# Kernel tuning notes

Hardware: AMD Instinct MI355X
Metric: run time of the kernel (lower is better)

Reference implementation:

```python
import jax, jax.numpy as jnp
import numpy as np

B, L, DIN, D = 16, 1024, 512, 1024  # batch, l_max, input_dim, d_model
ORDER = 2


def setup_inputs() -> dict:
    key = jax.random.key(0)
    ks = jax.random.split(key, 8)
    n = lambda i, shape, sc: jax.random.normal(ks[i], shape, dtype=jnp.float32) * sc
    return {
        "x": n(0, (B, L, DIN), 1.0),
        # project_in (Linear since input_dim != output_dim)
        "Wp": n(1, (DIN, D), DIN ** -0.5),
        "bp": jnp.zeros((D,), jnp.float32),
        # hyena in_proj -> (order+1)*d channels
        "W_in": n(2, (D, 3 * D), D ** -0.5),
        "b_in": jnp.zeros((3 * D,), jnp.float32),
        # depthwise causal short conv, kernel 3
        "short_w": n(3, (3 * D, 1, 3), 0.5),
        "short_b": jnp.zeros((3 * D,), jnp.float32),
        # implicit long filters (materialized) + per-channel skip bias
        "k_filt": n(4, (ORDER, L, D), 0.02),
        "D_bias": n(5, (ORDER, D), 1.0),
        # hyena out_proj
        "W_out": n(6, (D, D), D ** -0.5),
        "b_out": jnp.zeros((D,), jnp.float32),
    }


def _fftconv(v, k, d_bias):
    # v: [B, L, d], k: [L, d] -> causal long conv via zero-padded FFT + skip
    n = 2 * v.shape[1]
    vf = jnp.fft.rfft(v.astype(jnp.float32), n=n, axis=1)
    kf = jnp.fft.rfft(k.astype(jnp.float32), n=n, axis=0)
    y = jnp.fft.irfft(vf * kf[None], n=n, axis=1)[:, : v.shape[1]]
    return (y + v * d_bias).astype(v.dtype)


def reference(x, Wp, bp, W_in, b_in, short_w, short_b, k_filt, D_bias, W_out, b_out):
    u = x @ Wp + bp                      # [B, L, D] project_in
    u = u @ W_in + b_in                  # [B, L, 3D]
    # depthwise causal short conv over sequence
    uc = jnp.transpose(u, (0, 2, 1))     # [B, 3D, L]
    uc = jax.lax.conv_general_dilated(
        uc, short_w, window_strides=(1,), padding=[(2, 0)],
        feature_group_count=3 * D, dimension_numbers=("NCH", "OIH", "NCH"),
    )[..., :L] + short_b[None, :, None]
    uc = jnp.transpose(uc, (0, 2, 1))    # [B, L, 3D]
    x1, x2, v = jnp.split(uc, 3, axis=-1)
    # Hyena recurrence: gate then long FFT conv, order=2
    v = _fftconv(v * x2, k_filt[0], D_bias[0])
    v = _fftconv(v * x1, k_filt[1], D_bias[1])
    return v @ W_out + b_out             # [B, L, D]
```

## Files before the change

kernel.cpp:

```cpp
#include <hip/hip_runtime.h>

#define BATCH 16
#define LSEQ 1024
#define DIN 512
#define DMODEL 1024
#define D3 3072
#define KCP 1064

typedef __attribute__((ext_vector_type(4))) float f32x4;
typedef __attribute__((ext_vector_type(8))) short bf16x8;

static __device__ __forceinline__ ushort f2bf(float f) {
    uint u = __float_as_uint(f);
    return (ushort)((u + 0x7FFFu + ((u >> 16) & 1u)) >> 16);
}
static __device__ __forceinline__ float bf2f(ushort h) {
    return __uint_as_float(((uint)h) << 16);
}

#define GLD16(ldst, gsrc)                                                        \
    __builtin_amdgcn_global_load_lds(                                            \
        (const __attribute__((address_space(1))) void*)(gsrc),                   \
        (__attribute__((address_space(3))) void*)(ldst), 16, 0, 0)

template <typename OutT, bool HAS_BIAS>
__global__ __launch_bounds__(256) void gemm_mfma(const ushort* __restrict__ A,
                                                 const ushort* __restrict__ Bt,
                                                 const float* __restrict__ bias,
                                                 OutT* __restrict__ C,
                                                 int M, int N, int K) {
    __shared__ ushort Als[2][128 * 32];
    __shared__ ushort Bls[2][128 * 32];
    int nwg = gridDim.x * gridDim.y;
    int bid = blockIdx.y * gridDim.x + blockIdx.x;
    bid = (bid & 7) * (nwg >> 3) + (bid >> 3);
    int n0 = (bid % gridDim.x) * 128, m0 = (bid / gridDim.x) * 128;
    int t = threadIdx.x;
    int w = t >> 6, l = t & 63;
    int wm = w & 1, wn = w >> 1;
    f32x4 acc[4][4] = {};

    int rowA = t >> 2;
    int kb = (t & 3) * 8;
    const ushort* gA0 = A + (size_t)(m0 + rowA) * K + kb;
    const ushort* gA1 = gA0 + (size_t)64 * K;
    const ushort* gB0 = Bt + (size_t)(n0 + rowA) * K + kb;
    const ushort* gB1 = gB0 + (size_t)64 * K;
    int so = 512 * w;

    int aoff = (wm * 64 + (l & 15)) * 32 + (l >> 4) * 8;
    int boff = (wn * 64 + (l & 15)) * 32 + (l >> 4) * 8;

    GLD16(&Als[0][so], gA0);
    GLD16(&Als[0][2048 + so], gA1);
    GLD16(&Bls[0][so], gB0);
    GLD16(&Bls[0][2048 + so], gB1);
    GLD16(&Als[1][so], gA0 + 32);
    GLD16(&Als[1][2048 + so], gA1 + 32);
    GLD16(&Bls[1][so], gB0 + 32);
    GLD16(&Bls[1][2048 + so], gB1 + 32);

    int cur = 0;
    for (int k0 = 0; k0 < K; k0 += 32) {
        if (k0 + 32 < K)
            asm volatile("s_waitcnt vmcnt(4)" ::: "memory");
        else
            asm volatile("s_waitcnt vmcnt(0)" ::: "memory");
        __builtin_amdgcn_s_barrier();
        __builtin_amdgcn_sched_barrier(0);
        bf16x8 af[4], bg[4];
#pragma unroll
        for (int i = 0; i < 4; i++) af[i] = *(const bf16x8*)&Als[cur][aoff + i * 512];
#pragma unroll
        for (int j = 0; j < 4; j++) bg[j] = *(const bf16x8*)&Bls[cur][boff + j * 512];
#pragma unroll
        for (int i = 0; i < 4; i++)
#pragma unroll
            for (int j = 0; j < 4; j++)
                acc[i][j] = __builtin_amdgcn_mfma_f32_16x16x32_bf16(af[i], bg[j],
                                                                    acc[i][j], 0, 0, 0);
        asm volatile("s_waitcnt lgkmcnt(0)" ::: "memory");
        __builtin_amdgcn_sched_barrier(0);
        __builtin_amdgcn_s_barrier();
        if (k0 + 64 < K) {
            GLD16(&Als[cur][so], gA0 + k0 + 64);
            GLD16(&Als[cur][2048 + so], gA1 + k0 + 64);
            GLD16(&Bls[cur][so], gB0 + k0 + 64);
            GLD16(&Bls[cur][2048 + so], gB1 + k0 + 64);
        }
        cur ^= 1;
    }

#pragma unroll
    for (int j = 0; j < 4; j++) {
        int col = n0 + wn * 64 + 16 * j + (l & 15);
        float bv = HAS_BIAS ? bias[col] : 0.f;
#pragma unroll
        for (int i = 0; i < 4; i++) {
            int row0 = m0 + wm * 64 + 16 * i + (l >> 4) * 4;
#pragma unroll
            for (int r = 0; r < 4; r++) {
                float v = acc[i][j][r] + bv;
                if constexpr (sizeof(OutT) == 2)
                    C[(size_t)(row0 + r) * N + col] = (OutT)f2bf(v);
                else
                    C[(size_t)(row0 + r) * N + col] = (OutT)v;
            }
        }
    }
}

__global__ __launch_bounds__(512, 2) void conv_mfma(const ushort* __restrict__ At,
                                                    const ushort* __restrict__ X1t,
                                                    const float* __restrict__ kt,
                                                    const float* __restrict__ Db,
                                                    ushort* __restrict__ V2t, int nb) {
    __shared__ ushort a_lds[16 * 1024];
    __shared__ ushort kc[8 * KCP];
    int d = blockIdx.x;
    int tid = threadIdx.x;
    int w = tid >> 6, l = tid & 63;
    int lr = l & 15, lq = l >> 4;

    {
        int b = tid >> 5, s = tid & 31;
        const ushort* g = At + ((size_t)b * DMODEL + d) * LSEQ + s * 32;
#pragma unroll
        for (int j = 0; j < 4; j++) {
            uint4 v = {0u, 0u, 0u, 0u};
            if (b < nb) v = *(const uint4*)(g + 8 * j);
            int byte = (b * 1024 + s * 32 + 8 * j) * 2;
            *(uint4*)((char*)a_lds + (byte ^ (b << 4))) = v;
        }
    }

    int p = (7 - lr) & 7;
    int v0 = 1023 - lr + 8 * lq - p;
    int a_base = lr * 2048 + lq * 16;
    int swz = lr << 4;
    int tL0 = 2 * w, tF0 = 2 * w + 1;
    int tL1 = 30 - 2 * w, tF1 = 31 - 2 * w;

#define AFB(BLK) (*(const bf16x8*)((const char*)a_lds + ((a_base + 64 * (BLK)) ^ swz)))
#define MF(AF, B, AC) AC = __builtin_amdgcn_mfma_f32_16x16x32_bf16(AF, B, AC, 0, 0, 0)

    for (int o = 0; o < 2; o++) {
        const float* krow = kt + ((size_t)o * DMODEL + d) * LSEQ;
        for (int idx = tid; idx < 8 * KCP; idx += 512) {
            int pp = idx / KCP;
            int u = idx - pp * KCP;
            int ki = 1023 - u - pp;
            kc[idx] = f2bf((ki >= 0) ? krow[ki] : 0.f);
        }
        __syncthreads();

        f32x4 aL0l = {}, aL0h = {}, aF0l = {}, aF0h = {};
        f32x4 aL1l = {}, aL1h = {}, aF1l = {}, aF1h = {};
        const char* kbp = (const char*)kc + ((size_t)p * KCP + v0) * 2;
        bf16x8 hold0, hold1;
        {
            bf16x8 b0 = *(const bf16x8*)(kbp);
            bf16x8 b1 = *(const bf16x8*)(kbp - 32);
            __builtin_amdgcn_s_setprio(1);
            bf16x8 f0 = AFB(tF0);
            MF(f0, b0, aF0l); MF(f0, b1, aF0h);
            hold0 = AFB(tL0);
            MF(hold0, b0, aL0l); MF(hold0, b1, aL0h);
            bf16x8 f1 = AFB(tF1);
            MF(f1, b0, aF1l); MF(f1, b1, aF1h);
            hold1 = AFB(tL1);
            MF(hold1, b0, aL1l); MF(hold1, b1, aL1h);
            __builtin_amdgcn_s_setprio(0);
        }
        for (int m = 1; m < 32; m++) {
            bf16x8 b0 = *(const bf16x8*)(kbp - 64 * m);
            bf16x8 b1 = *(const bf16x8*)(kbp - 64 * m - 32);
            __builtin_amdgcn_s_setprio(1);
            if (m <= tF0) { MF(hold0, b0, aF0l); MF(hold0, b1, aF0h); }
            if (m <= tL0) {
                hold0 = AFB(tL0 - m);
                MF(hold0, b0, aL0l); MF(hold0, b1, aL0h);
            }
            if (m <= tF1) { MF(hold1, b0, aF1l); MF(hold1, b1, aF1h); }
            if (m <= tL1) {
                hold1 = AFB(tL1 - m);
                MF(hold1, b0, aL1l); MF(hold1, b1, aL1h);
            }
            __builtin_amdgcn_s_setprio(0);
        }
        float db = Db[o * DMODEL + d];
        __syncthreads();
#define CEPI(TI, AC, H)                                                        \
        {                                                                      \
            _Pragma("unroll")                                                  \
            for (int r = 0; r < 4; r++) {                                      \
                int t2 = 32 * (TI) + 16 * (H) + lr;                            \
                int b = lq * 4 + r;                                            \
                int ab = ((b * 1024 + t2) * 2) ^ (b << 4);                     \
                float a0v = bf2f(*(const ushort*)((const char*)a_lds + ab));   \
                float y = (AC)[r] + a0v * db;                                  \
                if (o == 0) {                                                  \
                    float g = (b < nb)                                         \
                        ? bf2f(X1t[((size_t)b * DMODEL + d) * LSEQ + t2]) : 0.f; \
                    y *= g;                                                    \
                }                                                              \
                *(ushort*)((char*)a_lds + ab) = f2bf(y);                       \
            }                                                                  \
        }
        CEPI(tL0, aL0l, 0) CEPI(tL0, aL0h, 1)
        CEPI(tF0, aF0l, 0) CEPI(tF0, aF0h, 1)
        CEPI(tL1, aL1l, 0) CEPI(tL1, aL1h, 1)
        CEPI(tF1, aF1l, 0) CEPI(tF1, aF1h, 1)
#undef CEPI
    }
#undef AFB
#undef MF
    __syncthreads();
    {
        int b = tid >> 5, s = tid & 31;
        if (b < nb) {
            ushort* g = V2t + ((size_t)b * DMODEL + d) * LSEQ + s * 32;
#pragma unroll
            for (int j = 0; j < 4; j++) {
                int byte = (b * 1024 + s * 32 + 8 * j) * 2;
                uint4 v = *(const uint4*)((const char*)a_lds + (byte ^ (b << 4)));
                *(uint4*)(g + 8 * j) = v;
            }
        }
    }
}

__global__ void cvt_bf16(const float* __restrict__ in, ushort* __restrict__ out, int n4) {
    int i = blockIdx.x * blockDim.x + threadIdx.x;
    if (i >= n4) return;
    float4 v = *(const float4*)&in[4 * i];
    uint2 pk;
    pk.x = (uint)f2bf(v.x) | ((uint)f2bf(v.y) << 16);
    pk.y = (uint)f2bf(v.z) | ((uint)f2bf(v.w) << 16);
    *(uint2*)&out[4 * i] = pk;
}

__global__ void transpose_cvt(const float* __restrict__ in, ushort* __restrict__ out,
                              int R, int C) {
    __shared__ float tile[32][33];
    int c0 = blockIdx.x * 32, r0 = blockIdx.y * 32;
    int tx = threadIdx.x, ty = threadIdx.y;
#pragma unroll
    for (int i = 0; i < 4; i++)
        tile[ty + 8 * i][tx] = in[(size_t)(r0 + ty + 8 * i) * C + c0 + tx];
    __syncthreads();
#pragma unroll
    for (int i = 0; i < 4; i++)
        out[(size_t)(c0 + ty + 8 * i) * R + r0 + tx] = f2bf(tile[tx][ty + 8 * i]);
}

__global__ __launch_bounds__(256) void transpose_b16(const ushort* __restrict__ in,
                                                     ushort* __restrict__ out) {
    __shared__ uint tile[64][33];
    int t0 = blockIdx.x * 64, d0 = blockIdx.y * 64, b = blockIdx.z;
    int i = threadIdx.x;
    const ushort* ip = in + (size_t)b * DMODEL * LSEQ;
    ushort* op = out + (size_t)b * LSEQ * DMODEL;
    int dl = i >> 5, cu = i & 31;
#pragma unroll
    for (int j = 0; j < 8; j++)
        tile[dl + 8 * j][cu] =
            *(const uint*)&ip[(size_t)(d0 + dl + 8 * j) * LSEQ + t0 + 2 * cu];
    __syncthreads();
    int du = i & 31, tb = i >> 5;
#pragma unroll
    for (int j = 0; j < 8; j++) {
        int tl = tb + 8 * j;
        uint lo = (tile[2 * du][tl >> 1] >> (16 * (tl & 1))) & 0xFFFFu;
        uint hi = (tile[2 * du + 1][tl >> 1] >> (16 * (tl & 1))) & 0xFFFFu;
        *(uint*)&op[(size_t)(t0 + tl) * DMODEL + d0 + 2 * du] = lo | (hi << 16);
    }
}

__global__ void bias_fuse(const float* __restrict__ bp, const float* __restrict__ W_in,
                          const float* __restrict__ b_in, float* __restrict__ bf) {
    int n = blockIdx.x * blockDim.x + threadIdx.x;
    float s = b_in[n];
    for (int k = 0; k < DMODEL; k++) s += bp[k] * W_in[(size_t)k * D3 + n];
    bf[n] = s;
}

__global__ void transpose_k(const float* __restrict__ kf, float* __restrict__ kt) {
    __shared__ float tile[32][33];
    int s0 = blockIdx.x * 32, d0 = blockIdx.y * 32, o = blockIdx.z;
    int tx = threadIdx.x, ty = threadIdx.y;
#pragma unroll
    for (int i = 0; i < 4; i++)
        tile[ty + 8 * i][tx] = kf[((size_t)o * LSEQ + s0 + ty + 8 * i) * DMODEL + d0 + tx];
    __syncthreads();
#pragma unroll
    for (int i = 0; i < 4; i++)
        kt[((size_t)o * DMODEL + d0 + ty + 8 * i) * LSEQ + s0 + tx] = tile[tx][ty + 8 * i];
}

__global__ __launch_bounds__(256) void shortconv_gate(const ushort* __restrict__ UC,
                                                      const float* __restrict__ sw,
                                                      const float* __restrict__ sb,
                                                      ushort* __restrict__ At,
                                                      ushort* __restrict__ X1t) {
    __shared__ uint tin[34][33];
    __shared__ ushort oA[64][34];
    __shared__ ushort oX[64][34];
    int t0 = blockIdx.x * 32, c0 = blockIdx.y * 64, b = blockIdx.z;
    int tx = threadIdx.x, ty = threadIdx.y;
    float2 res[3][4];
#pragma unroll
    for (int g = 0; g < 3; g++) {
        int ch = g * DMODEL + c0 + 2 * tx;
        __syncthreads();
        for (int r = ty; r < 34; r += 8) {
            int t = t0 + r - 2;
            tin[r][tx] = (t >= 0)
                ? *(const uint*)&UC[((size_t)b * LSEQ + t) * D3 + ch] : 0u;
        }
        __syncthreads();
        float w00 = sw[ch * 3 + 0], w01 = sw[ch * 3 + 1], w02 = sw[ch * 3 + 2];
        float w10 = sw[ch * 3 + 3], w11 = sw[ch * 3 + 4], w12 = sw[ch * 3 + 5];
        float bb0 = sb[ch], bb1 = sb[ch + 1];
#pragma unroll
        for (int i = 0; i < 4; i++) {
            int r = ty + 8 * i + 2;
            uint u0 = tin[r - 2][tx], u1 = tin[r - 1][tx], u2 = tin[r][tx];
            res[g][i].x = w00 * bf2f((ushort)u0) + w01 * bf2f((ushort)u1) +
                          w02 * bf2f((ushort)u2) + bb0;
            res[g][i].y = w10 * bf2f((ushort)(u0 >> 16)) + w11 * bf2f((ushort)(u1 >> 16)) +
                          w12 * bf2f((ushort)(u2 >> 16)) + bb1;
        }
    }
#pragma unroll
    for (int i = 0; i < 4; i++) {
        int t = ty + 8 * i;
        oA[2 * tx][t]     = f2bf(res[2][i].x * res[1][i].x);
        oA[2 * tx + 1][t] = f2bf(res[2][i].y * res[1][i].y);
        oX[2 * tx][t]     = f2bf(res[0][i].x);
        oX[2 * tx + 1][t] = f2bf(res[0][i].y);
    }
    __syncthreads();
    int li = ty * 32 + tx;
    int row = li >> 2, cu0 = (li & 3) * 4;
    ushort* gA = At  + ((size_t)b * DMODEL + c0 + row) * LSEQ + t0;
    ushort* gX = X1t + ((size_t)b * DMODEL + c0 + row) * LSEQ + t0;
#pragma unroll
    for (int j = 0; j < 4; j++) {
        int cu = cu0 + j;
        uint av = (uint)oA[row][2 * cu] | ((uint)oA[row][2 * cu + 1] << 16);
        uint xv = (uint)oX[row][2 * cu] | ((uint)oX[row][2 * cu + 1] << 16);
        *(uint*)&gA[2 * cu] = av;
        *(uint*)&gX[2 * cu] = xv;
    }
}

extern "C" void kernel_launch(void* const* d_in, const int* in_sizes, int n_in,
                              void* d_out, int out_size, void* d_ws, size_t ws_size,
                              hipStream_t stream) {
    (void)in_sizes; (void)n_in; (void)out_size;
    const float* x    = (const float*)d_in[0];
    const float* Wp   = (const float*)d_in[1];
    const float* bp   = (const float*)d_in[2];
    const float* W_in = (const float*)d_in[3];
    const float* b_in = (const float*)d_in[4];
    const float* sw   = (const float*)d_in[5];
    const float* sb   = (const float*)d_in[6];
    const float* kf   = (const float*)d_in[7];
    const float* Db   = (const float*)d_in[8];
    const float* Wout = (const float*)d_in[9];
    const float* bout = (const float*)d_in[10];
    float* out = (float*)d_out;

    char* ws = (char*)d_ws;
    ushort* Wf_t   = (ushort*)(ws);
    float*  bfv    = (float*)(ws + 3145728);
    float*  kt     = (float*)(ws + 3162112);
    ushort* Wout_t = (ushort*)(ws + 11550720);
    const size_t PB = 13647872;

    const size_t XB  = 1048576;
    const size_t ATB = 2097152;
    const size_t X1B = 2097152;
    const size_t UCB = 6291456;
    const size_t V2B = 2097152;
    const size_t PREPB = 7340032;

    int cb = 1, cf = 1;
    {
        bool ok = false;
        for (int tcb = 16; tcb >= 1 && !ok; tcb >>= 1) {
            for (int tcf = tcb; tcf >= 1; tcf >>= 1) {
                size_t ucreg = (size_t)tcf * UCB;
                size_t v2need = (size_t)2 * tcb * V2B;
                if (ucreg < v2need) ucreg = v2need;
                if (ucreg < PREPB) ucreg = PREPB;
                size_t need = PB + (size_t)tcb * (XB + ATB + X1B) + ucreg;
                if (need <= ws_size) { cb = tcb; cf = tcf; ok = true; break; }
            }
        }
    }

    ushort* x_bf = (ushort*)(ws + PB);
    ushort* Atb  = (ushort*)(ws + PB + (size_t)cb * XB);
    ushort* X1tb = (ushort*)(ws + PB + (size_t)cb * (XB + ATB));
    char*   ucrg = ws + PB + (size_t)cb * (XB + ATB + X1B);
    ushort* UC   = (ushort*)ucrg;
    ushort* V2t  = (ushort*)ucrg;
    ushort* V2   = (ushort*)(ucrg + (size_t)cb * V2B);
    ushort* W_inT = (ushort*)ucrg;
    ushort* Wp_bf = (ushort*)(ucrg + 6291456);

    transpose_cvt<<<dim3(96, 32), dim3(32, 8), 0, stream>>>(W_in, W_inT, DMODEL, D3);
    cvt_bf16<<<512, 256, 0, stream>>>(Wp, Wp_bf, DIN * DMODEL / 4);
    gemm_mfma<ushort, false><<<dim3(4, 24), 256, 0, stream>>>(W_inT, Wp_bf, nullptr,
                                                              Wf_t, D3, DIN, DMODEL);
    bias_fuse<<<D3 / 256, 256, 0, stream>>>(bp, W_in, b_in, bfv);
    transpose_cvt<<<dim3(32, 32), dim3(32, 8), 0, stream>>>(Wout, Wout_t, DMODEL, DMODEL);
    transpose_k<<<dim3(32, 32, 2), dim3(32, 8), 0, stream>>>(kf, kt);

    for (int b0 = 0; b0 < BATCH; b0 += cb) {
        cvt_bf16<<<cb * LSEQ * DIN / 1024, 256, 0, stream>>>(
            x + (size_t)b0 * LSEQ * DIN, x_bf, cb * LSEQ * DIN / 4);
        for (int f0 = 0; f0 < cb; f0 += cf) {
            gemm_mfma<ushort, true><<<dim3(24, cf * 8), 256, 0, stream>>>(
                x_bf + (size_t)f0 * LSEQ * DIN, Wf_t, bfv, UC, cf * LSEQ, D3, DIN);
            shortconv_gate<<<dim3(32, 16, cf), dim3(32, 8), 0, stream>>>(
                UC, sw, sb, Atb + (size_t)f0 * DMODEL * LSEQ,
                X1tb + (size_t)f0 * DMODEL * LSEQ);
        }
        conv_mfma<<<DMODEL, 512, 0, stream>>>(Atb, X1tb, kt, Db, V2t, cb);
        transpose_b16<<<dim3(16, 16, cb), dim3(256), 0, stream>>>(V2t, V2);
        gemm_mfma<float, true><<<dim3(8, cb * 8), 256, 0, stream>>>(
            V2, Wout_t, bout, out + (size_t)b0 * LSEQ * DMODEL, cb * LSEQ, DMODEL, DMODEL);
    }
}
```

Baseline: 415.7 us.

## Enlarge GEMM tile to 256x128 with 8 waves and split bias fusion reduction

The MFMA GEMM now uses 512 threads with a 256x128 output tile, so each workgroup shares one B tile across twice as many A rows. This reuses loaded B data more and halves the number of workgroups, at the cost of more LDS and fewer blocks to spread across CUs. The bias fusion kernel, which had each thread loop serially over 1024 k values, is split into a partial-sum kernel over 8 k-chunks plus a small reduction kernel, exposing more parallelism. The workspace budget grows slightly to hold the partial sums.

Measured after the change: 340.2 us. -18.2%, faster.

```diff
diff --git a/kernel.cpp b/kernel.cpp
--- a/kernel.cpp
+++ b/kernel.cpp
@@ -24,46 +24,44 @@
         (__attribute__((address_space(3))) void*)(ldst), 16, 0, 0)
 
 template <typename OutT, bool HAS_BIAS>
-__global__ __launch_bounds__(256) void gemm_mfma(const ushort* __restrict__ A,
+__global__ __launch_bounds__(512) void gemm_mfma(const ushort* __restrict__ A,
                                                  const ushort* __restrict__ Bt,
                                                  const float* __restrict__ bias,
                                                  OutT* __restrict__ C,
                                                  int M, int N, int K) {
-    __shared__ ushort Als[2][128 * 32];
+    __shared__ ushort Als[2][256 * 32];
     __shared__ ushort Bls[2][128 * 32];
     int nwg = gridDim.x * gridDim.y;
     int bid = blockIdx.y * gridDim.x + blockIdx.x;
     bid = (bid & 7) * (nwg >> 3) + (bid >> 3);
-    int n0 = (bid % gridDim.x) * 128, m0 = (bid / gridDim.x) * 128;
+    int n0 = (bid % gridDim.x) * 128, m0 = (bid / gridDim.x) * 256;
     int t = threadIdx.x;
     int w = t >> 6, l = t & 63;
-    int wm = w & 1, wn = w >> 1;
+    int wm = w >> 1, wn = w & 1;
     f32x4 acc[4][4] = {};
 
-    int rowA = t >> 2;
-    int kb = (t & 3) * 8;
-    const ushort* gA0 = A + (size_t)(m0 + rowA) * K + kb;
-    const ushort* gA1 = gA0 + (size_t)64 * K;
-    const ushort* gB0 = Bt + (size_t)(n0 + rowA) * K + kb;
-    const ushort* gB1 = gB0 + (size_t)64 * K;
-    int so = 512 * w;
+    int arow0 = 32 * w + (l >> 2);
+    int kpart = (l & 3) * 8;
+    const ushort* gA0 = A + (size_t)(m0 + arow0) * K + kpart;
+    const ushort* gA1 = gA0 + (size_t)16 * K;
+    const ushort* gB0 = Bt + (size_t)(n0 + 16 * w + (l >> 2)) * K + kpart;
+    int soA = 1024 * w;
+    int soB = 512 * w;
 
     int aoff = (wm * 64 + (l & 15)) * 32 + (l >> 4) * 8;
     int boff = (wn * 64 + (l & 15)) * 32 + (l >> 4) * 8;
 
-    GLD16(&Als[0][so], gA0);
-    GLD16(&Als[0][2048 + so], gA1);
-    GLD16(&Bls[0][so], gB0);
-    GLD16(&Bls[0][2048 + so], gB1);
-    GLD16(&Als[1][so], gA0 + 32);
-    GLD16(&Als[1][2048 + so], gA1 + 32);
-    GLD16(&Bls[1][so], gB0 + 32);
-    GLD16(&Bls[1][2048 + so], gB1 + 32);
+    GLD16(&Als[0][soA], gA0);
+    GLD16(&Als[0][soA + 512], gA1);
+    GLD16(&Bls[0][soB], gB0);
+    GLD16(&Als[1][soA], gA0 + 32);
+    GLD16(&Als[1][soA + 512], gA1 + 32);
+    GLD16(&Bls[1][soB], gB0 + 32);
 
     int cur = 0;
     for (int k0 = 0; k0 < K; k0 += 32) {
         if (k0 + 32 < K)
-            asm volatile("s_waitcnt vmcnt(4)" ::: "memory");
+            asm volatile("s_waitcnt vmcnt(3)" ::: "memory");
         else
             asm volatile("s_waitcnt vmcnt(0)" ::: "memory");
         __builtin_amdgcn_s_barrier();
@@ -83,10 +81,9 @@
         __builtin_amdgcn_sched_barrier(0);
         __builtin_amdgcn_s_barrier();
         if (k0 + 64 < K) {
-            GLD16(&Als[cur][so], gA0 + k0 + 64);
-            GLD16(&Als[cur][2048 + so], gA1 + k0 + 64);
-            GLD16(&Bls[cur][so], gB0 + k0 + 64);
-            GLD16(&Bls[cur][2048 + so], gB1 + k0 + 64);
+            GLD16(&Als[cur][soA], gA0 + k0 + 64);
+            GLD16(&Als[cur][soA + 512], gA1 + k0 + 64);
+            GLD16(&Bls[cur][soB], gB0 + k0 + 64);
         }
         cur ^= 1;
     }
@@ -277,11 +274,22 @@
     }
 }
 
-__global__ void bias_fuse(const float* __restrict__ bp, const float* __restrict__ W_in,
-                          const float* __restrict__ b_in, float* __restrict__ bf) {
-    int n = blockIdx.x * blockDim.x + threadIdx.x;
+__global__ void bias_fuse_part(const float* __restrict__ bp,
+                               const float* __restrict__ W_in,
+                               float* __restrict__ partial) {
+    int n = blockIdx.x * 256 + threadIdx.x;
+    int k0 = blockIdx.y * 128;
+    float s = 0.f;
+    for (int k = k0; k < k0 + 128; k++) s += bp[k] * W_in[(size_t)k * D3 + n];
+    partial[(size_t)blockIdx.y * D3 + n] = s;
+}
+__global__ void bias_fuse_red(const float* __restrict__ partial,
+                              const float* __restrict__ b_in,
+                              float* __restrict__ bf) {
+    int n = blockIdx.x * 256 + threadIdx.x;
     float s = b_in[n];
-    for (int k = 0; k < DMODEL; k++) s += bp[k] * W_in[(size_t)k * D3 + n];
+#pragma unroll
+    for (int j = 0; j < 8; j++) s += partial[(size_t)j * D3 + n];
     bf[n] = s;
 }
 
@@ -384,7 +392,7 @@
     const size_t X1B = 2097152;
     const size_t UCB = 6291456;
     const size_t V2B = 2097152;
-    const size_t PREPB = 7340032;
+    const size_t PREPB = 7471104;
 
     int cb = 1, cf = 1;
     {
@@ -410,12 +418,14 @@
     ushort* V2   = (ushort*)(ucrg + (size_t)cb * V2B);
     ushort* W_inT = (ushort*)ucrg;
     ushort* Wp_bf = (ushort*)(ucrg + 6291456);
+    float*  bfp   = (float*)(ucrg + 7340032);
 
     transpose_cvt<<<dim3(96, 32), dim3(32, 8), 0, stream>>>(W_in, W_inT, DMODEL, D3);
     cvt_bf16<<<512, 256, 0, stream>>>(Wp, Wp_bf, DIN * DMODEL / 4);
-    gemm_mfma<ushort, false><<<dim3(4, 24), 256, 0, stream>>>(W_inT, Wp_bf, nullptr,
+    gemm_mfma<ushort, false><<<dim3(4, 12), 512, 0, stream>>>(W_inT, Wp_bf, nullptr,
                                                               Wf_t, D3, DIN, DMODEL);
-    bias_fuse<<<D3 / 256, 256, 0, stream>>>(bp, W_in, b_in, bfv);
+    bias_fuse_part<<<dim3(12, 8), 256, 0, stream>>>(bp, W_in, bfp);
+    bias_fuse_red<<<12, 256, 0, stream>>>(bfp, b_in, bfv);
     transpose_cvt<<<dim3(32, 32), dim3(32, 8), 0, stream>>>(Wout, Wout_t, DMODEL, DMODEL);
     transpose_k<<<dim3(32, 32, 2), dim3(32, 8), 0, stream>>>(kf, kt);
 
@@ -423,7 +433,7 @@
         cvt_bf16<<<cb * LSEQ * DIN / 1024, 256, 0, stream>>>(
             x + (size_t)b0 * LSEQ * DIN, x_bf, cb * LSEQ * DIN / 4);
         for (int f0 = 0; f0 < cb; f0 += cf) {
-            gemm_mfma<ushort, true><<<dim3(24, cf * 8), 256, 0, stream>>>(
+            gemm_mfma<ushort, true><<<dim3(24, cf * 4), 512, 0, stream>>>(
                 x_bf + (size_t)f0 * LSEQ * DIN, Wf_t, bfv, UC, cf * LSEQ, D3, DIN);
             shortconv_gate<<<dim3(32, 16, cf), dim3(32, 8), 0, stream>>>(
                 UC, sw, sb, Atb + (size_t)f0 * DMODEL * LSEQ,
@@ -431,7 +441,7 @@
         }
         conv_mfma<<<DMODEL, 512, 0, stream>>>(Atb, X1tb, kt, Db, V2t, cb);
         transpose_b16<<<dim3(16, 16, cb), dim3(256), 0, stream>>>(V2t, V2);
-        gemm_mfma<float, true><<<dim3(8, cb * 8), 256, 0, stream>>>(
+        gemm_mfma<float, true><<<dim3(8, cb * 4), 512, 0, stream>>>(
             V2, Wout_t, bout, out + (size_t)b0 * LSEQ * DMODEL, cb * LSEQ, DMODEL, DMODEL);
     }
 }
```
